# Optimization experiments

Measured on AMD Instinct MI355X. Metric: run time of the kernel, lower is better.

Reference implementation:

```python
import jax, jax.numpy as jnp
import numpy as np

D_DYN = 256    # dynamic_dim
D_STAT = 64    # static_dim
U_DIM = 48     # config.model.u_dim
N_OBS = 80     # num_prod*2 + num_inj = 32*2 + 16
T = 128        # rollout steps
B = 2048       # batch


def setup_inputs() -> dict:
    key = jax.random.key(0)
    k = jax.random.split(key, 8)
    z_dyn = jax.random.normal(k[0], (B, D_DYN), dtype=jnp.float32)
    z_static = jax.random.normal(k[1], (B, D_STAT), dtype=jnp.float32)
    dt = jnp.ones((1,), dtype=jnp.float32) * 0.05
    U = jax.random.normal(k[2], (T, B, U_DIM), dtype=jnp.float32)
    # learned params, initialized as in the torch module
    eig_raw = jnp.zeros((D_DYN,), dtype=jnp.float32)
    V = jnp.eye(D_DYN, dtype=jnp.float32) + jax.random.normal(k[3], (D_DYN, D_DYN), dtype=jnp.float32) * 0.01
    L = jax.random.normal(k[4], (D_DYN, U_DIM), dtype=jnp.float32) * (1.0 / np.sqrt(U_DIM))
    C = jax.random.normal(k[5], (N_OBS, D_DYN), dtype=jnp.float32) * (1.0 / np.sqrt(D_DYN))
    Dm = jax.random.normal(k[6], (N_OBS, U_DIM), dtype=jnp.float32) * (1.0 / np.sqrt(U_DIM))
    return {"z_dyn": z_dyn, "z_static": z_static, "dt": dt, "U": U,
            "eig_raw": eig_raw, "V": V, "L": L, "C": C, "Dm": Dm}


def reference(z_dyn, z_static, dt, U, eig_raw, V, L, C, Dm):
    # Stable Koopman operator: K = V diag(sigmoid(eig_raw)*0.99) V^{-1}
    eigvals = jax.nn.sigmoid(eig_raw) * 0.99
    K = (V * eigvals[None, :]) @ jnp.linalg.inv(V)  # [d, d]
    KT, LT, CT, DT = K.T, L.T, C.T, Dm.T
    dts = dt[0]

    def step(z, ut):
        ut_dt = ut * dts                 # [B, u_dim]
        z = z @ KT + ut_dt @ LT          # [B, d]
        y = z @ CT + ut_dt @ DT          # [B, n_obs]
        return z, (z, y)

    _, (Z, Y) = jax.lax.scan(step, z_dyn, U)
    return Z, Y  # [T, B, d], [T, B, n_obs]
```

## Files before the change

kernel.cpp:

```cpp
#include <hip/hip_runtime.h>

#define D_   256
#define UD_  48
#define NO_  80
#define T_   128
#define B_   2048

typedef __bf16 bf16x8 __attribute__((ext_vector_type(8)));
typedef float  f32x4  __attribute__((ext_vector_type(4)));
typedef unsigned short ushort_t;

static __device__ __forceinline__ ushort_t f2bf(float f){
  return __builtin_bit_cast(ushort_t, (__bf16)f);
}
static __device__ __forceinline__ float bf2f(ushort_t u){
  union { unsigned int i; float f; } c; c.i = ((unsigned int)u) << 16; return c.f;
}
static __device__ __forceinline__ f32x4 mfma16(bf16x8 a, bf16x8 b, f32x4 c){
  return __builtin_amdgcn_mfma_f32_16x16x32_bf16(a, b, c, 0, 0, 0);
}


__global__ void k_init(const float* __restrict__ V, const float* __restrict__ eig,
                       float* __restrict__ Xa, float* __restrict__ lam){
  const int i = blockIdx.x, j = threadIdx.x;
  Xa[i*D_ + j] = (i == j ? 2.0f : 0.0f) - V[i*D_ + j];
  if (j == 0) lam[i] = 0.99f / (1.0f + expf(-eig[i]));
}

__global__ void k_mm_mul(const float* __restrict__ A, const float* __restrict__ B,
                         float* __restrict__ Cm){
  const int i = blockIdx.x, j = threadIdx.x;
  const float* Ar = A + i*D_;
  float a0=0.f,a1=0.f,a2=0.f,a3=0.f;
  #pragma unroll 4
  for (int k = 0; k < D_; k += 4){
    a0 += Ar[k+0] * B[(k+0)*D_ + j];
    a1 += Ar[k+1] * B[(k+1)*D_ + j];
    a2 += Ar[k+2] * B[(k+2)*D_ + j];
    a3 += Ar[k+3] * B[(k+3)*D_ + j];
  }
  Cm[i*D_ + j] = (a0+a1)+(a2+a3);
}

__global__ void k_mm_upd(const float* __restrict__ X, const float* __restrict__ Tm,
                         float* __restrict__ Xn){
  const int i = blockIdx.x, j = threadIdx.x;
  const float* Xr = X + i*D_;
  float a0=0.f,a1=0.f,a2=0.f,a3=0.f;
  #pragma unroll 4
  for (int k = 0; k < D_; k += 4){
    a0 += Xr[k+0] * Tm[(k+0)*D_ + j];
    a1 += Xr[k+1] * Tm[(k+1)*D_ + j];
    a2 += Xr[k+2] * Tm[(k+2)*D_ + j];
    a3 += Xr[k+3] * Tm[(k+3)*D_ + j];
  }
  Xn[i*D_ + j] = 2.0f*Xr[j] - ((a0+a1)+(a2+a3));
}

__global__ void k_prep1(const float* __restrict__ Vinv, const float* __restrict__ V,
                        const float* __restrict__ Lm, const float* __restrict__ Cmat,
                        const float* __restrict__ dt,
                        float* __restrict__ VinvT, float* __restrict__ Lw,
                        float* __restrict__ Cw, float* __restrict__ dVd){
  const int bid = blockIdx.x, tid = threadIdx.x;
  if (bid < 256){
    VinvT[tid*D_ + bid] = Vinv[bid*D_ + tid];
    if (tid == bid){ float v = V[bid*D_ + bid]; dVd[bid] = v - bf2f(f2bf(v)); }
  } else if (bid < 512){
    const int i = bid - 256;
    if (tid < UD_){
      float acc = 0.f;
      #pragma unroll 4
      for (int j = 0; j < D_; ++j) acc += Vinv[i*D_ + j] * Lm[j*UD_ + tid];
      Lw[i*UD_ + tid] = acc * dt[0];
    }
  } else {
    const int n = bid - 512;
    float acc = 0.f;
    #pragma unroll 4
    for (int j = 0; j < D_; ++j) acc += Cmat[n*D_ + j] * V[j*D_ + tid];
    Cw[n*D_ + tid] = acc;
  }
}

__global__ void k_prep2(const float* __restrict__ z0, const float* __restrict__ VinvT,
                        const float* __restrict__ Lw,
                        ushort_t* __restrict__ Wchk, ushort_t* __restrict__ Lws){
  __shared__ float zr[8][256];
  const int bid = blockIdx.x, tid = threadIdx.x;
  if (bid < 256){
    const int b0 = bid * 8;
    #pragma unroll
    for (int r = 0; r < 8; ++r) zr[r][tid] = z0[(size_t)(b0+r)*D_ + tid];
    __syncthreads();
    float acc[8] = {0.f,0.f,0.f,0.f,0.f,0.f,0.f,0.f};
    #pragma unroll 4
    for (int j = 0; j < D_; ++j){
      const float vj = VinvT[j*D_ + tid];
      #pragma unroll
      for (int r = 0; r < 8; ++r) acc[r] += zr[r][j] * vj;
    }
    #pragma unroll
    for (int r = 0; r < 8; ++r)
      Wchk[(size_t)(b0+r)*D_ + tid] = f2bf(acc[r]);
    return;
  }
  const int f = bid - 256;
  if (tid >= 64) return;
  const int l = tid, lm = l & 15, lh = l >> 4;
  const int it = f >> 1, kc2 = f & 1;
  const int ig = it*16 + lm;
  #pragma unroll
  for (int j = 0; j < 8; ++j){
    const int k = 32*kc2 + 4*lh + (j & 3) + 16*(j >> 2);
    Lws[(f*64 + l)*8 + j] = f2bf(k < UD_ ? Lw[ig*UD_ + k] : 0.f);
  }
}

__global__ void k_packA(const float* __restrict__ V, const float* __restrict__ Cw,
                        const float* __restrict__ Dmat, const float* __restrict__ dt,
                        ushort_t* __restrict__ Af){
  const int mt = blockIdx.x / 10, kc = blockIdx.x % 10;
  const int l = threadIdx.x, lm = l & 15, lh = l >> 4;
  const float dts = dt[0];
  #pragma unroll
  for (int j = 0; j < 8; ++j){
    const int k = 32*kc + 4*lh + (j & 3) + 16*(j >> 2);
    float val = 0.f;
    if (mt < 16){
      if (kc < 8) val = V[(mt*16 + lm)*D_ + k];
    } else {
      const int n = (mt - 16)*16 + lm;
      if (kc < 8) val = Cw[n*D_ + k];
      else { const int ku = k - 256; if (ku < UD_) val = dts * Dmat[n*UD_ + ku]; }
    }
    Af[((size_t)(mt*10 + kc)*64 + l)*8 + j] = f2bf(val);
  }
}

#define SCAN_STEP(UA, UB, UC, TT) do {                                          \
  union { ushort_t us[8]; bf16x8 v; } c0, c1;                                   \
  c0.us[0]=f2bf((UA).x); c0.us[1]=f2bf((UA).y); c0.us[2]=f2bf((UA).z); c0.us[3]=f2bf((UA).w); \
  c0.us[4]=f2bf((UB).x); c0.us[5]=f2bf((UB).y); c0.us[6]=f2bf((UB).z); c0.us[7]=f2bf((UB).w); \
  c1.us[0]=f2bf((UC).x); c1.us[1]=f2bf((UC).y); c1.us[2]=f2bf((UC).z); c1.us[3]=f2bf((UC).w); \
  c1.us[4]=0; c1.us[5]=0; c1.us[6]=0; c1.us[7]=0;                               \
  _Pragma("unroll")                                                             \
  for (int q = 0; q < 2; ++q){                                                  \
    f32x4 acc = {0.f,0.f,0.f,0.f};                                              \
    acc = mfma16(lwf[q*2+0], c0.v, acc);                                        \
    acc = mfma16(lwf[q*2+1], c1.v, acc);                                        \
    _Pragma("unroll")                                                           \
    for (int r = 0; r < 4; ++r) w[q*4+r] = lamr[q*4+r]*w[q*4+r] + acc[r];       \
  }                                                                             \
  if ((((TT) & 7) == 7) && ((TT) < T_-1)){                                      \
    const int c2 = ((TT)+1) >> 3;                                               \
    _Pragma("unroll")                                                           \
    for (int q = 0; q < 2; ++q){                                                \
      const int i = (itb+q)*16 + 4*lh;                                          \
      ushort4 o; o.x=f2bf(w[q*4+0]); o.y=f2bf(w[q*4+1]); o.z=f2bf(w[q*4+2]); o.w=f2bf(w[q*4+3]); \
      *(ushort4*)(Wchk + ((size_t)c2*B_ + row)*D_ + i) = o;                     \
    }                                                                           \
  }                                                                             \
} while(0)

__global__ void __launch_bounds__(256) k_scan(const float* __restrict__ U,
    const ushort_t* __restrict__ Lws, const float* __restrict__ lam,
    ushort_t* __restrict__ Wchk){
  const int tid = threadIdx.x;
  const int wid = tid >> 6, l = tid & 63;
  const int lm = l & 15, lh = l >> 4;
  const int bq = blockIdx.x >> 1, ih = blockIdx.x & 1;
  const int b0 = bq * 16;
  const int row = b0 + lm;
  const int itb = ih*8 + wid*2;

  bf16x8 lwf[4];
  #pragma unroll
  for (int q = 0; q < 2; ++q)
    #pragma unroll
    for (int c = 0; c < 2; ++c)
      lwf[q*2 + c] = *(const bf16x8*)(Lws + ((size_t)(((itb+q)*2 + c)*64 + l))*8);

  float lamr[8], w[8];
  #pragma unroll
  for (int q = 0; q < 2; ++q){
    const int i = (itb+q)*16 + 4*lh;
    const float4 lv = *(const float4*)&lam[i];
    const ushort4 wu = *(const ushort4*)(Wchk + (size_t)row*D_ + i);
    lamr[q*4+0]=lv.x; lamr[q*4+1]=lv.y; lamr[q*4+2]=lv.z; lamr[q*4+3]=lv.w;
    w[q*4+0]=bf2f(wu.x); w[q*4+1]=bf2f(wu.y); w[q*4+2]=bf2f(wu.z); w[q*4+3]=bf2f(wu.w);
  }

  const size_t TS = (size_t)B_ * UD_;
  const float* Urow = U + (size_t)row * UD_;
  float4 Aa, Ab, Ac, Ba, Bb, Bc;
  Aa = *(const float4*)&Urow[4*lh]; Ab = *(const float4*)&Urow[16+4*lh]; Ac = *(const float4*)&Urow[32+4*lh];
  { const float* Up = Urow + TS;
    Ba = *(const float4*)&Up[4*lh]; Bb = *(const float4*)&Up[16+4*lh]; Bc = *(const float4*)&Up[32+4*lh]; }

  #pragma unroll 1
  for (int tt = 0; tt < 64; ++tt){
    const int t0 = 2*tt;
    SCAN_STEP(Aa, Ab, Ac, t0);
    if (t0 + 2 < T_){
      const float* Up = Urow + (size_t)(t0+2)*TS;
      Aa = *(const float4*)&Up[4*lh]; Ab = *(const float4*)&Up[16+4*lh]; Ac = *(const float4*)&Up[32+4*lh];
    }
    SCAN_STEP(Ba, Bb, Bc, t0+1);
    if (t0 + 3 < T_){
      const float* Up = Urow + (size_t)(t0+3)*TS;
      Ba = *(const float4*)&Up[4*lh]; Bb = *(const float4*)&Up[16+4*lh]; Bc = *(const float4*)&Up[32+4*lh];
    }
  }
}

__global__ void __launch_bounds__(256) k_fused(
    const float* __restrict__ U, const ushort_t* __restrict__ Af,
    const ushort_t* __restrict__ Lws, const float* __restrict__ lam,
    const float* __restrict__ dVd, const ushort_t* __restrict__ Wchk,
    float* __restrict__ outZ, float* __restrict__ outY){
  __shared__ __align__(16) ushort_t AfZhL[8*8*512];
  __shared__ __align__(16) ushort_t LwsL[32*512];
  __shared__ __align__(16) ushort_t AfYhL[30*512];
  __shared__ __align__(16) float    trbZ[4][16][68];
  __shared__ __align__(16) float    dVdL[128];
  __shared__ __align__(16) float    lamL[256];

  const int tid = threadIdx.x;
  const int bid = blockIdx.x;
  const int h  = bid >> 9;
  const int ch = bid & 15;
  const int bq = (bid >> 4) & 31;
  const int wid = tid >> 6, l = tid & 63;
  const int lm = l & 15, lh = l >> 4;
  const int col0 = bq*64 + wid*16;
  const int col = col0 + lm;

  {
    const uint4* gsrc = (const uint4*)Af;
    uint4* dz = (uint4*)AfZhL;
    #pragma unroll
    for (int r = 0; r < 16; ++r){
      const int i = r*256 + tid;
      const int f = i >> 6, l4 = i & 63;
      const int mi8 = f >> 3, kc = f & 7;
      dz[i] = gsrc[(size_t)((h*8 + mi8)*10 + kc)*64 + l4];
    }
    uint4* dy = (uint4*)AfYhL;
    const int nY = h ? 1280 : 1920;
    const int sb = 16 + (h ? 3 : 0);
    #pragma unroll
    for (int r = 0; r < 8; ++r){
      const int i = r*256 + tid;
      if (i < nY){
        const int f = i >> 6, l4 = i & 63;
        const int myl = f / 10, j = f % 10;
        dy[i] = gsrc[(size_t)((sb + myl)*10 + j)*64 + l4];
      }
    }
    const uint4* ls = (const uint4*)Lws;
    uint4* ld = (uint4*)LwsL;
    #pragma unroll
    for (int r = 0; r < 8; ++r) ld[r*256 + tid] = ls[r*256 + tid];
    if (tid < 32) ((float4*)dVdL)[tid] = ((const float4*)(dVd + h*128))[tid];
    else if (tid < 96) ((float4*)lamL)[tid-32] = ((const float4*)lam)[tid-32];
  }

  float w[64];
  #pragma unroll
  for (int kc = 0; kc < 8; ++kc)
    #pragma unroll
    for (int hh = 0; hh < 2; ++hh){
      const int i = 32*kc + 16*hh + 4*lh;
      const ushort4 wu = *(const ushort4*)(Wchk + ((size_t)ch*B_ + col)*D_ + i);
      const int e = 8*kc + 4*hh;
      w[e+0]=bf2f(wu.x); w[e+1]=bf2f(wu.y); w[e+2]=bf2f(wu.z); w[e+3]=bf2f(wu.w);
    }

  const size_t TS = (size_t)B_ * UD_;
  const float* Ucol = U + (size_t)col * UD_;
  float4 ua, ub, uc;
  {
    const float* Ut = Ucol + (size_t)(ch*8)*TS;
    ua = *(const float4*)&Ut[4*lh]; ub = *(const float4*)&Ut[16+4*lh]; uc = *(const float4*)&Ut[32+4*lh];
  }

  __syncthreads();

#define ZLOOP(HH)                                                               \
  { float* zbase = outZ + ((size_t)t*B_ + col0)*D_ + (HH)*128;                  \
    _Pragma("unroll")                                                           \
    for (int g = 0; g < 2; ++g){                                                \
      _Pragma("unroll")                                                         \
      for (int mi = 0; mi < 4; ++mi){                                           \
        const int mi8 = g*4 + mi;                                               \
        f32x4 acc = {0.f,0.f,0.f,0.f};                                          \
        _Pragma("unroll")                                                       \
        for (int kc = 0; kc < 8; ++kc){                                         \
          const bf16x8 af = *(const bf16x8*)&AfZhL[((mi8*8+kc)*64 + l)*8];      \
          acc = mfma16(af, wfr[kc], acc);                                       \
        }                                                                       \
        const float4 dv = *(const float4*)&dVdL[mi8*16 + 4*lh];                 \
        acc[0] += dv.x * (float)wfr[((HH)*8+mi8)>>1][0 + 4*(mi8&1)];            \
        acc[1] += dv.y * (float)wfr[((HH)*8+mi8)>>1][1 + 4*(mi8&1)];            \
        acc[2] += dv.z * (float)wfr[((HH)*8+mi8)>>1][2 + 4*(mi8&1)];            \
        acc[3] += dv.w * (float)wfr[((HH)*8+mi8)>>1][3 + 4*(mi8&1)];            \
        *(float4*)&trbZ[wid][lm][mi*16 + 4*lh] = make_float4(acc[0],acc[1],acc[2],acc[3]); \
      }                                                                         \
      __builtin_amdgcn_wave_barrier();                                          \
      _Pragma("unroll")                                                         \
      for (int j = 0; j < 4; ++j){                                              \
        const int r_ = j*4 + (l >> 4), c16 = l & 15;                            \
        const float4 v = *(const float4*)&trbZ[wid][r_][4*c16];                 \
        *(float4*)&zbase[(size_t)r_*D_ + g*64 + 4*c16] = v;                     \
      }                                                                         \
      __builtin_amdgcn_wave_barrier();                                          \
    } }

#define YLOOP(COFF, NMY)                                                        \
  { float* yrow = outY + ((size_t)t*B_ + col)*NO_ + (COFF);                     \
    _Pragma("unroll")                                                           \
    for (int my = 0; my < (NMY); ++my){                                         \
      f32x4 acc = {0.f,0.f,0.f,0.f};                                            \
      _Pragma("unroll")                                                         \
      for (int kc = 0; kc < 8; ++kc){                                           \
        const bf16x8 af = *(const bf16x8*)&AfYhL[((my*10+kc)*64 + l)*8];        \
        acc = mfma16(af, wfr[kc], acc);                                         \
      }                                                                         \
      { const bf16x8 af8 = *(const bf16x8*)&AfYhL[((my*10+8)*64 + l)*8];        \
        const bf16x8 af9 = *(const bf16x8*)&AfYhL[((my*10+9)*64 + l)*8];        \
        acc = mfma16(af8, uf0, acc); acc = mfma16(af9, uf1, acc); }             \
      *(float4*)&yrow[my*16 + 4*lh] = make_float4(acc[0],acc[1],acc[2],acc[3]); \
    } }

  #pragma unroll 1
  for (int s = 0; s < 8; ++s){
    const int t = ch*8 + s;
    bf16x8 uf0, uf1;
    {
      union { ushort_t us[8]; bf16x8 v; } cv;
      cv.us[0]=f2bf(ua.x); cv.us[1]=f2bf(ua.y); cv.us[2]=f2bf(ua.z); cv.us[3]=f2bf(ua.w);
      cv.us[4]=f2bf(ub.x); cv.us[5]=f2bf(ub.y); cv.us[6]=f2bf(ub.z); cv.us[7]=f2bf(ub.w);
      uf0 = cv.v;
      cv.us[0]=f2bf(uc.x); cv.us[1]=f2bf(uc.y); cv.us[2]=f2bf(uc.z); cv.us[3]=f2bf(uc.w);
      cv.us[4]=0; cv.us[5]=0; cv.us[6]=0; cv.us[7]=0;
      uf1 = cv.v;
    }
    if (s < 7){
      const float* Ut = Ucol + (size_t)(t+1)*TS;
      ua = *(const float4*)&Ut[4*lh]; ub = *(const float4*)&Ut[16+4*lh]; uc = *(const float4*)&Ut[32+4*lh];
    }
    #pragma unroll
    for (int it = 0; it < 16; ++it){
      const bf16x8 a0 = *(const bf16x8*)&LwsL[((it*2+0)*64 + l)*8];
      const bf16x8 a1 = *(const bf16x8*)&LwsL[((it*2+1)*64 + l)*8];
      const float4 lv = *(const float4*)&lamL[32*(it>>1) + 16*(it&1) + 4*lh];
      f32x4 acc = {0.f,0.f,0.f,0.f};
      acc = mfma16(a0, uf0, acc);
      acc = mfma16(a1, uf1, acc);
      const int e0 = 8*(it>>1) + 4*(it&1);
      w[e0+0] = lv.x*w[e0+0] + acc[0];
      w[e0+1] = lv.y*w[e0+1] + acc[1];
      w[e0+2] = lv.z*w[e0+2] + acc[2];
      w[e0+3] = lv.w*w[e0+3] + acc[3];
    }
    bf16x8 wfr[8];
    #pragma unroll
    for (int kc = 0; kc < 8; ++kc){
      union { ushort_t us[8]; bf16x8 v; } cv;
      #pragma unroll
      for (int j = 0; j < 8; ++j) cv.us[j] = f2bf(w[8*kc + j]);
      wfr[kc] = cv.v;
    }
    if (h == 0){
      ZLOOP(0);
      YLOOP(0, 3);
    } else {
      ZLOOP(1);
      YLOOP(48, 2);
    }
  }
#undef ZLOOP
#undef YLOOP
}

extern "C" void kernel_launch(void* const* d_in, const int* in_sizes, int n_in,
                              void* d_out, int out_size, void* d_ws, size_t ws_size,
                              hipStream_t stream){
  const float* z0  = (const float*)d_in[0];
  const float* dt  = (const float*)d_in[2];
  const float* U   = (const float*)d_in[3];
  const float* eig = (const float*)d_in[4];
  const float* V   = (const float*)d_in[5];
  const float* L   = (const float*)d_in[6];
  const float* C   = (const float*)d_in[7];
  const float* Dm  = (const float*)d_in[8];
  float* outZ = (float*)d_out;
  float* outY = outZ + (size_t)T_*B_*D_;

  char* ws = (char*)d_ws;
  float* Xa    = (float*)(ws + 0);
  float* Xb    = (float*)(ws + 262144);
  float* Tt    = (float*)(ws + 524288);
  float* Lw    = (float*)(ws + 786432);
  float* Cw    = (float*)(ws + 835584);
  float* lam   = (float*)(ws + 917504);
  float* dVd   = (float*)(ws + 918528);
  ushort_t* Af   = (ushort_t*)(ws + 919552);
  ushort_t* Lws  = (ushort_t*)(ws + 1134592);
  ushort_t* Wchk = (ushort_t*)(ws + 1167360);
  if (ws_size < 17944576u) return;

  k_init<<<256,256,0,stream>>>(V, eig, Xa, lam);
  k_mm_mul<<<256,256,0,stream>>>(V, Xa, Tt);
  k_mm_upd<<<256,256,0,stream>>>(Xa, Tt, Xb);
  k_mm_mul<<<256,256,0,stream>>>(V, Xb, Tt);
  k_mm_upd<<<256,256,0,stream>>>(Xb, Tt, Xa);
  k_mm_mul<<<256,256,0,stream>>>(V, Xa, Tt);
  k_mm_upd<<<256,256,0,stream>>>(Xa, Tt, Xb);
  k_prep1<<<592,256,0,stream>>>(Xb, V, L, C, dt, Xa, Lw, Cw, dVd);
  k_prep2<<<288,256,0,stream>>>(z0, Xa, Lw, Wchk, Lws);
  k_packA<<<210,64,0,stream>>>(V, Cw, Dm, dt, Af);
  k_scan<<<256,256,0,stream>>>(U, Lws, lam, Wchk);
  k_fused<<<1024,256,0,stream>>>(U, Af, Lws, lam, dVd, Wchk, outZ, outY);
}
```

Before: 267.8 us.

## Merge preparation and scan kernels into one cooperative kernel with grid syncs

Eleven small preparation launches (Newton-Schulz inverse iterations, the projections, the packing and the chunked scan) become one cooperative kernel that separates phases with grid.sync(). This removes launch gaps and tail idle time between the many tiny dependent kernels. The fused kernel's block-to-work mapping is also reordered so the two halves are interleaved, and the Y output rows are split differently between halves (4 vs 1 tiles instead of 3 vs 2). Risks are the cost of grid-wide barriers and an uneven load between the two halves in the fused kernel.

```diff
diff --git a/kernel.cpp b/kernel.cpp
--- a/kernel.cpp
+++ b/kernel.cpp
@@ -1,4 +1,7 @@
 #include <hip/hip_runtime.h>
+#include <hip/hip_cooperative_groups.h>
+
+namespace cg = cooperative_groups;
 
 #define D_   256
 #define UD_  48
@@ -21,123 +24,23 @@
 }
 
 
-__global__ void k_init(const float* __restrict__ V, const float* __restrict__ eig,
-                       float* __restrict__ Xa, float* __restrict__ lam){
-  const int i = blockIdx.x, j = threadIdx.x;
-  Xa[i*D_ + j] = (i == j ? 2.0f : 0.0f) - V[i*D_ + j];
-  if (j == 0) lam[i] = 0.99f / (1.0f + expf(-eig[i]));
-}
-
-__global__ void k_mm_mul(const float* __restrict__ A, const float* __restrict__ B,
-                         float* __restrict__ Cm){
-  const int i = blockIdx.x, j = threadIdx.x;
-  const float* Ar = A + i*D_;
-  float a0=0.f,a1=0.f,a2=0.f,a3=0.f;
-  #pragma unroll 4
-  for (int k = 0; k < D_; k += 4){
-    a0 += Ar[k+0] * B[(k+0)*D_ + j];
-    a1 += Ar[k+1] * B[(k+1)*D_ + j];
-    a2 += Ar[k+2] * B[(k+2)*D_ + j];
-    a3 += Ar[k+3] * B[(k+3)*D_ + j];
-  }
-  Cm[i*D_ + j] = (a0+a1)+(a2+a3);
-}
-
-__global__ void k_mm_upd(const float* __restrict__ X, const float* __restrict__ Tm,
-                         float* __restrict__ Xn){
-  const int i = blockIdx.x, j = threadIdx.x;
-  const float* Xr = X + i*D_;
-  float a0=0.f,a1=0.f,a2=0.f,a3=0.f;
-  #pragma unroll 4
-  for (int k = 0; k < D_; k += 4){
-    a0 += Xr[k+0] * Tm[(k+0)*D_ + j];
-    a1 += Xr[k+1] * Tm[(k+1)*D_ + j];
-    a2 += Xr[k+2] * Tm[(k+2)*D_ + j];
-    a3 += Xr[k+3] * Tm[(k+3)*D_ + j];
-  }
-  Xn[i*D_ + j] = 2.0f*Xr[j] - ((a0+a1)+(a2+a3));
-}
-
-__global__ void k_prep1(const float* __restrict__ Vinv, const float* __restrict__ V,
-                        const float* __restrict__ Lm, const float* __restrict__ Cmat,
-                        const float* __restrict__ dt,
-                        float* __restrict__ VinvT, float* __restrict__ Lw,
-                        float* __restrict__ Cw, float* __restrict__ dVd){
-  const int bid = blockIdx.x, tid = threadIdx.x;
-  if (bid < 256){
-    VinvT[tid*D_ + bid] = Vinv[bid*D_ + tid];
-    if (tid == bid){ float v = V[bid*D_ + bid]; dVd[bid] = v - bf2f(f2bf(v)); }
-  } else if (bid < 512){
-    const int i = bid - 256;
-    if (tid < UD_){
-      float acc = 0.f;
-      #pragma unroll 4
-      for (int j = 0; j < D_; ++j) acc += Vinv[i*D_ + j] * Lm[j*UD_ + tid];
-      Lw[i*UD_ + tid] = acc * dt[0];
-    }
-  } else {
-    const int n = bid - 512;
-    float acc = 0.f;
-    #pragma unroll 4
-    for (int j = 0; j < D_; ++j) acc += Cmat[n*D_ + j] * V[j*D_ + tid];
-    Cw[n*D_ + tid] = acc;
-  }
-}
-
-__global__ void k_prep2(const float* __restrict__ z0, const float* __restrict__ VinvT,
-                        const float* __restrict__ Lw,
-                        ushort_t* __restrict__ Wchk, ushort_t* __restrict__ Lws){
-  __shared__ float zr[8][256];
-  const int bid = blockIdx.x, tid = threadIdx.x;
-  if (bid < 256){
-    const int b0 = bid * 8;
-    #pragma unroll
-    for (int r = 0; r < 8; ++r) zr[r][tid] = z0[(size_t)(b0+r)*D_ + tid];
-    __syncthreads();
-    float acc[8] = {0.f,0.f,0.f,0.f,0.f,0.f,0.f,0.f};
-    #pragma unroll 4
-    for (int j = 0; j < D_; ++j){
-      const float vj = VinvT[j*D_ + tid];
-      #pragma unroll
-      for (int r = 0; r < 8; ++r) acc[r] += zr[r][j] * vj;
-    }
-    #pragma unroll
-    for (int r = 0; r < 8; ++r)
-      Wchk[(size_t)(b0+r)*D_ + tid] = f2bf(acc[r]);
-    return;
-  }
-  const int f = bid - 256;
-  if (tid >= 64) return;
-  const int l = tid, lm = l & 15, lh = l >> 4;
-  const int it = f >> 1, kc2 = f & 1;
-  const int ig = it*16 + lm;
-  #pragma unroll
-  for (int j = 0; j < 8; ++j){
-    const int k = 32*kc2 + 4*lh + (j & 3) + 16*(j >> 2);
-    Lws[(f*64 + l)*8 + j] = f2bf(k < UD_ ? Lw[ig*UD_ + k] : 0.f);
-  }
-}
-
-__global__ void k_packA(const float* __restrict__ V, const float* __restrict__ Cw,
-                        const float* __restrict__ Dmat, const float* __restrict__ dt,
-                        ushort_t* __restrict__ Af){
-  const int mt = blockIdx.x / 10, kc = blockIdx.x % 10;
-  const int l = threadIdx.x, lm = l & 15, lh = l >> 4;
-  const float dts = dt[0];
-  #pragma unroll
-  for (int j = 0; j < 8; ++j){
-    const int k = 32*kc + 4*lh + (j & 3) + 16*(j >> 2);
-    float val = 0.f;
-    if (mt < 16){
-      if (kc < 8) val = V[(mt*16 + lm)*D_ + k];
-    } else {
-      const int n = (mt - 16)*16 + lm;
-      if (kc < 8) val = Cw[n*D_ + k];
-      else { const int ku = k - 256; if (ku < UD_) val = dts * Dmat[n*UD_ + ku]; }
-    }
-    Af[((size_t)(mt*10 + kc)*64 + l)*8 + j] = f2bf(val);
-  }
-}
+#define NS_MUL(Ap, Bp, Cp) do {                                                 \
+  const float* Ar = (Ap) + bid*D_;                                              \
+  float a0=0.f,a1=0.f,a2=0.f,a3=0.f;                                            \
+  _Pragma("unroll 4")                                                           \
+  for (int k = 0; k < D_; k += 4){                                              \
+    a0 += Ar[k+0]*(Bp)[(k+0)*D_+tid]; a1 += Ar[k+1]*(Bp)[(k+1)*D_+tid];         \
+    a2 += Ar[k+2]*(Bp)[(k+2)*D_+tid]; a3 += Ar[k+3]*(Bp)[(k+3)*D_+tid]; }       \
+  (Cp)[bid*D_+tid] = (a0+a1)+(a2+a3); } while(0)
+
+#define NS_UPD(Xp, Tp, Xn) do {                                                 \
+  const float* Xr = (Xp) + bid*D_;                                              \
+  float a0=0.f,a1=0.f,a2=0.f,a3=0.f;                                            \
+  _Pragma("unroll 4")                                                           \
+  for (int k = 0; k < D_; k += 4){                                              \
+    a0 += Xr[k+0]*(Tp)[(k+0)*D_+tid]; a1 += Xr[k+1]*(Tp)[(k+1)*D_+tid];         \
+    a2 += Xr[k+2]*(Tp)[(k+2)*D_+tid]; a3 += Xr[k+3]*(Tp)[(k+3)*D_+tid]; }       \
+  (Xn)[bid*D_+tid] = 2.0f*Xr[tid] - ((a0+a1)+(a2+a3)); } while(0)
 
 #define SCAN_STEP(UA, UB, UC, TT) do {                                          \
   union { ushort_t us[8]; bf16x8 v; } c0, c1;                                   \
@@ -164,53 +67,140 @@
   }                                                                             \
 } while(0)
 
-__global__ void __launch_bounds__(256) k_scan(const float* __restrict__ U,
-    const ushort_t* __restrict__ Lws, const float* __restrict__ lam,
+__global__ void __launch_bounds__(256) k_prep(
+    const float* __restrict__ V, const float* __restrict__ eig,
+    const float* __restrict__ Lm, const float* __restrict__ Cmat,
+    const float* __restrict__ Dmat, const float* __restrict__ dt,
+    const float* __restrict__ z0, const float* __restrict__ U,
+    float* __restrict__ Xa, float* __restrict__ Xb, float* __restrict__ Tt,
+    float* __restrict__ Lw, float* __restrict__ Cw,
+    float* __restrict__ lam, float* __restrict__ dVd,
+    ushort_t* __restrict__ Af, ushort_t* __restrict__ Lws,
     ushort_t* __restrict__ Wchk){
-  const int tid = threadIdx.x;
-  const int wid = tid >> 6, l = tid & 63;
-  const int lm = l & 15, lh = l >> 4;
-  const int bq = blockIdx.x >> 1, ih = blockIdx.x & 1;
-  const int b0 = bq * 16;
-  const int row = b0 + lm;
-  const int itb = ih*8 + wid*2;
-
-  bf16x8 lwf[4];
-  #pragma unroll
-  for (int q = 0; q < 2; ++q)
-    #pragma unroll
-    for (int c = 0; c < 2; ++c)
-      lwf[q*2 + c] = *(const bf16x8*)(Lws + ((size_t)(((itb+q)*2 + c)*64 + l))*8);
-
-  float lamr[8], w[8];
-  #pragma unroll
-  for (int q = 0; q < 2; ++q){
-    const int i = (itb+q)*16 + 4*lh;
-    const float4 lv = *(const float4*)&lam[i];
-    const ushort4 wu = *(const ushort4*)(Wchk + (size_t)row*D_ + i);
-    lamr[q*4+0]=lv.x; lamr[q*4+1]=lv.y; lamr[q*4+2]=lv.z; lamr[q*4+3]=lv.w;
-    w[q*4+0]=bf2f(wu.x); w[q*4+1]=bf2f(wu.y); w[q*4+2]=bf2f(wu.z); w[q*4+3]=bf2f(wu.w);
-  }
-
-  const size_t TS = (size_t)B_ * UD_;
-  const float* Urow = U + (size_t)row * UD_;
-  float4 Aa, Ab, Ac, Ba, Bb, Bc;
-  Aa = *(const float4*)&Urow[4*lh]; Ab = *(const float4*)&Urow[16+4*lh]; Ac = *(const float4*)&Urow[32+4*lh];
-  { const float* Up = Urow + TS;
-    Ba = *(const float4*)&Up[4*lh]; Bb = *(const float4*)&Up[16+4*lh]; Bc = *(const float4*)&Up[32+4*lh]; }
-
-  #pragma unroll 1
-  for (int tt = 0; tt < 64; ++tt){
-    const int t0 = 2*tt;
-    SCAN_STEP(Aa, Ab, Ac, t0);
-    if (t0 + 2 < T_){
-      const float* Up = Urow + (size_t)(t0+2)*TS;
-      Aa = *(const float4*)&Up[4*lh]; Ab = *(const float4*)&Up[16+4*lh]; Ac = *(const float4*)&Up[32+4*lh];
-    }
-    SCAN_STEP(Ba, Bb, Bc, t0+1);
-    if (t0 + 3 < T_){
-      const float* Up = Urow + (size_t)(t0+3)*TS;
-      Ba = *(const float4*)&Up[4*lh]; Bb = *(const float4*)&Up[16+4*lh]; Bc = *(const float4*)&Up[32+4*lh];
+  __shared__ float zr[8][256];
+  cg::grid_group grid = cg::this_grid();
+  const int bid = blockIdx.x, tid = threadIdx.x;
+
+  Xa[bid*D_ + tid] = (bid == tid ? 2.0f : 0.0f) - V[bid*D_ + tid];
+  if (tid == 0) lam[bid] = 0.99f / (1.0f + expf(-eig[bid]));
+  grid.sync();
+  NS_MUL(V, Xa, Tt);  grid.sync();
+  NS_UPD(Xa, Tt, Xb); grid.sync();
+  NS_MUL(V, Xb, Tt);  grid.sync();
+  NS_UPD(Xb, Tt, Xa); grid.sync();
+  NS_MUL(V, Xa, Tt);  grid.sync();
+  NS_UPD(Xa, Tt, Xb); grid.sync();
+  {
+    Xa[tid*D_ + bid] = Xb[bid*D_ + tid];
+    if (tid == bid){ float v = V[bid*D_ + bid]; dVd[bid] = v - bf2f(f2bf(v)); }
+    if (tid < UD_){
+      float acc = 0.f;
+      #pragma unroll 4
+      for (int j = 0; j < D_; ++j) acc += Xb[bid*D_ + j] * Lm[j*UD_ + tid];
+      Lw[bid*UD_ + tid] = acc * dt[0];
+    }
+    if (bid < NO_){
+      float acc = 0.f;
+      #pragma unroll 4
+      for (int j = 0; j < D_; ++j) acc += Cmat[bid*D_ + j] * V[j*D_ + tid];
+      Cw[bid*D_ + tid] = acc;
+    }
+  }
+  grid.sync();
+  {
+    const int b0 = bid * 8;
+    #pragma unroll
+    for (int r = 0; r < 8; ++r) zr[r][tid] = z0[(size_t)(b0+r)*D_ + tid];
+    __syncthreads();
+    float acc[8] = {0.f,0.f,0.f,0.f,0.f,0.f,0.f,0.f};
+    #pragma unroll 4
+    for (int j = 0; j < D_; ++j){
+      const float vj = Xa[j*D_ + tid];
+      #pragma unroll
+      for (int r = 0; r < 8; ++r) acc[r] += zr[r][j] * vj;
+    }
+    #pragma unroll
+    for (int r = 0; r < 8; ++r)
+      Wchk[(size_t)(b0+r)*D_ + tid] = f2bf(acc[r]);
+
+    if (bid < 32 && tid < 64){
+      const int f = bid, l = tid, lm = l & 15, lh = l >> 4;
+      const int it = f >> 1, kc2 = f & 1;
+      const int ig = it*16 + lm;
+      #pragma unroll
+      for (int j = 0; j < 8; ++j){
+        const int k = 32*kc2 + 4*lh + (j & 3) + 16*(j >> 2);
+        Lws[(f*64 + l)*8 + j] = f2bf(k < UD_ ? Lw[ig*UD_ + k] : 0.f);
+      }
+    }
+    {
+      const int v = bid*4 + (tid >> 6);
+      if (v < 210){
+        const int mt = v / 10, kc = v % 10;
+        const int l = tid & 63, lm = l & 15, lh = l >> 4;
+        const float dts = dt[0];
+        #pragma unroll
+        for (int j = 0; j < 8; ++j){
+          const int k = 32*kc + 4*lh + (j & 3) + 16*(j >> 2);
+          float val = 0.f;
+          if (mt < 16){
+            if (kc < 8) val = V[(mt*16 + lm)*D_ + k];
+          } else {
+            const int n = (mt - 16)*16 + lm;
+            if (kc < 8) val = Cw[n*D_ + k];
+            else { const int ku = k - 256; if (ku < UD_) val = dts * Dmat[n*UD_ + ku]; }
+          }
+          Af[((size_t)(mt*10 + kc)*64 + l)*8 + j] = f2bf(val);
+        }
+      }
+    }
+  }
+  grid.sync();
+  {
+    const int wid = tid >> 6, l = tid & 63;
+    const int lm = l & 15, lh = l >> 4;
+    const int bq = bid >> 1, ih = bid & 1;
+    const int b0 = bq * 16;
+    const int row = b0 + lm;
+    const int itb = ih*8 + wid*2;
+
+    bf16x8 lwf[4];
+    #pragma unroll
+    for (int q = 0; q < 2; ++q)
+      #pragma unroll
+      for (int c = 0; c < 2; ++c)
+        lwf[q*2 + c] = *(const bf16x8*)(Lws + ((size_t)(((itb+q)*2 + c)*64 + l))*8);
+
+    float lamr[8], w[8];
+    #pragma unroll
+    for (int q = 0; q < 2; ++q){
+      const int i = (itb+q)*16 + 4*lh;
+      const float4 lv = *(const float4*)&lam[i];
+      const ushort4 wu = *(const ushort4*)(Wchk + (size_t)row*D_ + i);
+      lamr[q*4+0]=lv.x; lamr[q*4+1]=lv.y; lamr[q*4+2]=lv.z; lamr[q*4+3]=lv.w;
+      w[q*4+0]=bf2f(wu.x); w[q*4+1]=bf2f(wu.y); w[q*4+2]=bf2f(wu.z); w[q*4+3]=bf2f(wu.w);
+    }
+
+    const size_t TS = (size_t)B_ * UD_;
+    const float* Urow = U + (size_t)row * UD_;
+    float4 Aa, Ab, Ac, Ba, Bb, Bc;
+    Aa = *(const float4*)&Urow[4*lh]; Ab = *(const float4*)&Urow[16+4*lh]; Ac = *(const float4*)&Urow[32+4*lh];
+    { const float* Up = Urow + TS;
+      Ba = *(const float4*)&Up[4*lh]; Bb = *(const float4*)&Up[16+4*lh]; Bc = *(const float4*)&Up[32+4*lh]; }
+
+    #pragma unroll 1
+    for (int tt = 0; tt < 64; ++tt){
+      const int t0 = 2*tt;
+      SCAN_STEP(Aa, Ab, Ac, t0);
+      if (t0 + 2 < T_){
+        const float* Up = Urow + (size_t)(t0+2)*TS;
+        Aa = *(const float4*)&Up[4*lh]; Ab = *(const float4*)&Up[16+4*lh]; Ac = *(const float4*)&Up[32+4*lh];
+      }
+      SCAN_STEP(Ba, Bb, Bc, t0+1);
+      if (t0 + 3 < T_){
+        const float* Up = Urow + (size_t)(t0+3)*TS;
+        Ba = *(const float4*)&Up[4*lh]; Bb = *(const float4*)&Up[16+4*lh]; Bc = *(const float4*)&Up[32+4*lh];
+      }
     }
   }
 }
@@ -222,16 +212,16 @@
     float* __restrict__ outZ, float* __restrict__ outY){
   __shared__ __align__(16) ushort_t AfZhL[8*8*512];
   __shared__ __align__(16) ushort_t LwsL[32*512];
-  __shared__ __align__(16) ushort_t AfYhL[30*512];
+  __shared__ __align__(16) ushort_t AfYhL[40*512];
   __shared__ __align__(16) float    trbZ[4][16][68];
   __shared__ __align__(16) float    dVdL[128];
   __shared__ __align__(16) float    lamL[256];
 
   const int tid = threadIdx.x;
   const int bid = blockIdx.x;
-  const int h  = bid >> 9;
-  const int ch = bid & 15;
-  const int bq = (bid >> 4) & 31;
+  const int h  = bid & 1;
+  const int ch = (bid >> 1) & 15;
+  const int bq = bid >> 5;
   const int wid = tid >> 6, l = tid & 63;
   const int lm = l & 15, lh = l >> 4;
   const int col0 = bq*64 + wid*16;
@@ -248,10 +238,10 @@
       dz[i] = gsrc[(size_t)((h*8 + mi8)*10 + kc)*64 + l4];
     }
     uint4* dy = (uint4*)AfYhL;
-    const int nY = h ? 1280 : 1920;
-    const int sb = 16 + (h ? 3 : 0);
-    #pragma unroll
-    for (int r = 0; r < 8; ++r){
+    const int nY = h ? 640 : 2560;
+    const int sb = 16 + (h ? 4 : 0);
+    #pragma unroll
+    for (int r = 0; r < 10; ++r){
       const int i = r*256 + tid;
       if (i < nY){
         const int f = i >> 6, l4 = i & 63;
@@ -375,10 +365,10 @@
     }
     if (h == 0){
       ZLOOP(0);
-      YLOOP(0, 3);
+      YLOOP(0, 4);
     } else {
       ZLOOP(1);
-      YLOOP(48, 2);
+      YLOOP(64, 1);
     }
   }
 #undef ZLOOP
@@ -412,16 +402,15 @@
   ushort_t* Wchk = (ushort_t*)(ws + 1167360);
   if (ws_size < 17944576u) return;
 
-  k_init<<<256,256,0,stream>>>(V, eig, Xa, lam);
-  k_mm_mul<<<256,256,0,stream>>>(V, Xa, Tt);
-  k_mm_upd<<<256,256,0,stream>>>(Xa, Tt, Xb);
-  k_mm_mul<<<256,256,0,stream>>>(V, Xb, Tt);
-  k_mm_upd<<<256,256,0,stream>>>(Xb, Tt, Xa);
-  k_mm_mul<<<256,256,0,stream>>>(V, Xa, Tt);
-  k_mm_upd<<<256,256,0,stream>>>(Xa, Tt, Xb);
-  k_prep1<<<592,256,0,stream>>>(Xb, V, L, C, dt, Xa, Lw, Cw, dVd);
-  k_prep2<<<288,256,0,stream>>>(z0, Xa, Lw, Wchk, Lws);
-  k_packA<<<210,64,0,stream>>>(V, Cw, Dm, dt, Af);
-  k_scan<<<256,256,0,stream>>>(U, Lws, lam, Wchk);
+  {
+    void* args[] = {
+      (void*)&V, (void*)&eig, (void*)&L, (void*)&C, (void*)&Dm, (void*)&dt,
+      (void*)&z0, (void*)&U,
+      (void*)&Xa, (void*)&Xb, (void*)&Tt, (void*)&Lw, (void*)&Cw,
+      (void*)&lam, (void*)&dVd, (void*)&Af, (void*)&Lws, (void*)&Wchk
+    };
+    hipLaunchCooperativeKernel((const void*)k_prep, dim3(256), dim3(256),
+                               args, 0, stream);
+  }
   k_fused<<<1024,256,0,stream>>>(U, Af, Lws, lam, dVd, Wchk, outZ, outY);
 }
```

New measurement: 539.6 us. 2.01x slower.

## Process two timesteps per iteration to share A-fragment LDS loads across steps

Applied to the files above, without the earlier changes.

The fused kernel now advances the recurrence two timesteps per loop iteration and issues paired MFMAs that reuse each LDS-loaded A fragment for both steps. This halves LDS traffic for the Z and Y projection matrices. The block index mapping is changed so the two halves are interleaved across adjacent blocks, and the Y-output split between halves is rebalanced from 3/2 to 4/1 tiles. The cost is higher register pressure from the doubled fragments and accumulators, and the Y work split is now less even between halves.

```diff
diff --git a/kernel.cpp b/kernel.cpp
--- a/kernel.cpp
+++ b/kernel.cpp
@@ -222,16 +222,16 @@
     float* __restrict__ outZ, float* __restrict__ outY){
   __shared__ __align__(16) ushort_t AfZhL[8*8*512];
   __shared__ __align__(16) ushort_t LwsL[32*512];
-  __shared__ __align__(16) ushort_t AfYhL[30*512];
+  __shared__ __align__(16) ushort_t AfYhL[40*512];
   __shared__ __align__(16) float    trbZ[4][16][68];
   __shared__ __align__(16) float    dVdL[128];
   __shared__ __align__(16) float    lamL[256];
 
   const int tid = threadIdx.x;
   const int bid = blockIdx.x;
-  const int h  = bid >> 9;
-  const int ch = bid & 15;
-  const int bq = (bid >> 4) & 31;
+  const int h  = bid & 1;
+  const int ch = (bid >> 1) & 15;
+  const int bq = bid >> 5;
   const int wid = tid >> 6, l = tid & 63;
   const int lm = l & 15, lh = l >> 4;
   const int col0 = bq*64 + wid*16;
@@ -248,10 +248,10 @@
       dz[i] = gsrc[(size_t)((h*8 + mi8)*10 + kc)*64 + l4];
     }
     uint4* dy = (uint4*)AfYhL;
-    const int nY = h ? 1280 : 1920;
-    const int sb = 16 + (h ? 3 : 0);
-    #pragma unroll
-    for (int r = 0; r < 8; ++r){
+    const int nY = h ? 640 : 2560;
+    const int sb = 16 + (h ? 4 : 0);
+    #pragma unroll
+    for (int r = 0; r < 10; ++r){
       const int i = r*256 + tid;
       if (i < nY){
         const int f = i >> 6, l4 = i & 63;
@@ -280,105 +280,140 @@
 
   const size_t TS = (size_t)B_ * UD_;
   const float* Ucol = U + (size_t)col * UD_;
-  float4 ua, ub, uc;
+  float4 uaA, ubA, ucA, uaB, ubB, ucB;
   {
     const float* Ut = Ucol + (size_t)(ch*8)*TS;
-    ua = *(const float4*)&Ut[4*lh]; ub = *(const float4*)&Ut[16+4*lh]; uc = *(const float4*)&Ut[32+4*lh];
+    uaA = *(const float4*)&Ut[4*lh]; ubA = *(const float4*)&Ut[16+4*lh]; ucA = *(const float4*)&Ut[32+4*lh];
+    const float* Ut1 = Ut + TS;
+    uaB = *(const float4*)&Ut1[4*lh]; ubB = *(const float4*)&Ut1[16+4*lh]; ucB = *(const float4*)&Ut1[32+4*lh];
   }
 
   __syncthreads();
 
 #define ZLOOP(HH)                                                               \
-  { float* zbase = outZ + ((size_t)t*B_ + col0)*D_ + (HH)*128;                  \
+  { float* zA = outZ + ((size_t)t*B_ + col0)*D_ + (HH)*128;                     \
+    float* zB = zA + (size_t)B_*D_;                                             \
     _Pragma("unroll")                                                           \
-    for (int g = 0; g < 2; ++g){                                                \
+    for (int g = 0; g < 4; ++g){                                                \
       _Pragma("unroll")                                                         \
-      for (int mi = 0; mi < 4; ++mi){                                           \
-        const int mi8 = g*4 + mi;                                               \
-        f32x4 acc = {0.f,0.f,0.f,0.f};                                          \
+      for (int mi = 0; mi < 2; ++mi){                                           \
+        const int mi8 = g*2 + mi;                                               \
+        f32x4 aA = {0.f,0.f,0.f,0.f}, aB = {0.f,0.f,0.f,0.f};                   \
         _Pragma("unroll")                                                       \
         for (int kc = 0; kc < 8; ++kc){                                         \
           const bf16x8 af = *(const bf16x8*)&AfZhL[((mi8*8+kc)*64 + l)*8];      \
-          acc = mfma16(af, wfr[kc], acc);                                       \
+          aA = mfma16(af, wfrA[kc], aA);                                        \
+          aB = mfma16(af, wfrB[kc], aB);                                        \
         }                                                                       \
         const float4 dv = *(const float4*)&dVdL[mi8*16 + 4*lh];                 \
-        acc[0] += dv.x * (float)wfr[((HH)*8+mi8)>>1][0 + 4*(mi8&1)];            \
-        acc[1] += dv.y * (float)wfr[((HH)*8+mi8)>>1][1 + 4*(mi8&1)];            \
-        acc[2] += dv.z * (float)wfr[((HH)*8+mi8)>>1][2 + 4*(mi8&1)];            \
-        acc[3] += dv.w * (float)wfr[((HH)*8+mi8)>>1][3 + 4*(mi8&1)];            \
-        *(float4*)&trbZ[wid][lm][mi*16 + 4*lh] = make_float4(acc[0],acc[1],acc[2],acc[3]); \
+        _Pragma("unroll")                                                       \
+        for (int r = 0; r < 4; ++r){                                            \
+          aA[r] += ((const float*)&dv)[r] * (float)wfrA[(HH)*4+(mi8>>1)][r + 4*(mi8&1)]; \
+          aB[r] += ((const float*)&dv)[r] * (float)wfrB[(HH)*4+(mi8>>1)][r + 4*(mi8&1)]; \
+        }                                                                       \
+        *(float4*)&trbZ[wid][lm][mi*16 + 4*lh] = make_float4(aA[0],aA[1],aA[2],aA[3]); \
+        *(float4*)&trbZ[wid][lm][32 + mi*16 + 4*lh] = make_float4(aB[0],aB[1],aB[2],aB[3]); \
       }                                                                         \
       __builtin_amdgcn_wave_barrier();                                          \
       _Pragma("unroll")                                                         \
       for (int j = 0; j < 4; ++j){                                              \
-        const int r_ = j*4 + (l >> 4), c16 = l & 15;                            \
-        const float4 v = *(const float4*)&trbZ[wid][r_][4*c16];                 \
-        *(float4*)&zbase[(size_t)r_*D_ + g*64 + 4*c16] = v;                     \
+        const int stp = j >> 1, jr = (j & 1)*8;                                 \
+        const int r_ = jr + (l >> 3), c8 = l & 7;                               \
+        const float4 v = *(const float4*)&trbZ[wid][r_][stp*32 + 4*c8];         \
+        float* dst = stp ? zB : zA;                                             \
+        *(float4*)&dst[(size_t)r_*D_ + g*32 + 4*c8] = v;                        \
       }                                                                         \
       __builtin_amdgcn_wave_barrier();                                          \
     } }
 
 #define YLOOP(COFF, NMY)                                                        \
-  { float* yrow = outY + ((size_t)t*B_ + col)*NO_ + (COFF);                     \
+  { float* yA = outY + ((size_t)t*B_ + col)*NO_ + (COFF);                       \
+    float* yB = yA + (size_t)B_*NO_;                                            \
     _Pragma("unroll")                                                           \
     for (int my = 0; my < (NMY); ++my){                                         \
-      f32x4 acc = {0.f,0.f,0.f,0.f};                                            \
+      f32x4 aA = {0.f,0.f,0.f,0.f}, aB = {0.f,0.f,0.f,0.f};                     \
       _Pragma("unroll")                                                         \
       for (int kc = 0; kc < 8; ++kc){                                           \
         const bf16x8 af = *(const bf16x8*)&AfYhL[((my*10+kc)*64 + l)*8];        \
-        acc = mfma16(af, wfr[kc], acc);                                         \
+        aA = mfma16(af, wfrA[kc], aA);                                          \
+        aB = mfma16(af, wfrB[kc], aB);                                          \
       }                                                                         \
       { const bf16x8 af8 = *(const bf16x8*)&AfYhL[((my*10+8)*64 + l)*8];        \
         const bf16x8 af9 = *(const bf16x8*)&AfYhL[((my*10+9)*64 + l)*8];        \
-        acc = mfma16(af8, uf0, acc); acc = mfma16(af9, uf1, acc); }             \
-      *(float4*)&yrow[my*16 + 4*lh] = make_float4(acc[0],acc[1],acc[2],acc[3]); \
+        aA = mfma16(af8, ufA0, aA); aA = mfma16(af9, ufA1, aA);                 \
+        aB = mfma16(af8, ufB0, aB); aB = mfma16(af9, ufB1, aB); }               \
+      *(float4*)&yA[my*16 + 4*lh] = make_float4(aA[0],aA[1],aA[2],aA[3]);       \
+      *(float4*)&yB[my*16 + 4*lh] = make_float4(aB[0],aB[1],aB[2],aB[3]);       \
     } }
 
   #pragma unroll 1
-  for (int s = 0; s < 8; ++s){
-    const int t = ch*8 + s;
-    bf16x8 uf0, uf1;
+  for (int p = 0; p < 4; ++p){
+    const int t = ch*8 + 2*p;
+    bf16x8 ufA0, ufA1, ufB0, ufB1;
     {
       union { ushort_t us[8]; bf16x8 v; } cv;
-      cv.us[0]=f2bf(ua.x); cv.us[1]=f2bf(ua.y); cv.us[2]=f2bf(ua.z); cv.us[3]=f2bf(ua.w);
-      cv.us[4]=f2bf(ub.x); cv.us[5]=f2bf(ub.y); cv.us[6]=f2bf(ub.z); cv.us[7]=f2bf(ub.w);
-      uf0 = cv.v;
-      cv.us[0]=f2bf(uc.x); cv.us[1]=f2bf(uc.y); cv.us[2]=f2bf(uc.z); cv.us[3]=f2bf(uc.w);
+      cv.us[0]=f2bf(uaA.x); cv.us[1]=f2bf(uaA.y); cv.us[2]=f2bf(uaA.z); cv.us[3]=f2bf(uaA.w);
+      cv.us[4]=f2bf(ubA.x); cv.us[5]=f2bf(ubA.y); cv.us[6]=f2bf(ubA.z); cv.us[7]=f2bf(ubA.w);
+      ufA0 = cv.v;
+      cv.us[0]=f2bf(ucA.x); cv.us[1]=f2bf(ucA.y); cv.us[2]=f2bf(ucA.z); cv.us[3]=f2bf(ucA.w);
       cv.us[4]=0; cv.us[5]=0; cv.us[6]=0; cv.us[7]=0;
-      uf1 = cv.v;
-    }
-    if (s < 7){
-      const float* Ut = Ucol + (size_t)(t+1)*TS;
-      ua = *(const float4*)&Ut[4*lh]; ub = *(const float4*)&Ut[16+4*lh]; uc = *(const float4*)&Ut[32+4*lh];
-    }
-    #pragma unroll
-    for (int it = 0; it < 16; ++it){
-      const bf16x8 a0 = *(const bf16x8*)&LwsL[((it*2+0)*64 + l)*8];
-      const bf16x8 a1 = *(const bf16x8*)&LwsL[((it*2+1)*64 + l)*8];
-      const float4 lv = *(const float4*)&lamL[32*(it>>1) + 16*(it&1) + 4*lh];
-      f32x4 acc = {0.f,0.f,0.f,0.f};
-      acc = mfma16(a0, uf0, acc);
-      acc = mfma16(a1, uf1, acc);
-      const int e0 = 8*(it>>1) + 4*(it&1);
-      w[e0+0] = lv.x*w[e0+0] + acc[0];
-      w[e0+1] = lv.y*w[e0+1] + acc[1];
-      w[e0+2] = lv.z*w[e0+2] + acc[2];
-      w[e0+3] = lv.w*w[e0+3] + acc[3];
-    }
-    bf16x8 wfr[8];
-    #pragma unroll
-    for (int kc = 0; kc < 8; ++kc){
-      union { ushort_t us[8]; bf16x8 v; } cv;
+      ufA1 = cv.v;
+      cv.us[0]=f2bf(uaB.x); cv.us[1]=f2bf(uaB.y); cv.us[2]=f2bf(uaB.z); cv.us[3]=f2bf(uaB.w);
+      cv.us[4]=f2bf(ubB.x); cv.us[5]=f2bf(ubB.y); cv.us[6]=f2bf(ubB.z); cv.us[7]=f2bf(ubB.w);
+      ufB0 = cv.v;
+      cv.us[0]=f2bf(ucB.x); cv.us[1]=f2bf(ucB.y); cv.us[2]=f2bf(ucB.z); cv.us[3]=f2bf(ucB.w);
+      cv.us[4]=0; cv.us[5]=0; cv.us[6]=0; cv.us[7]=0;
+      ufB1 = cv.v;
+    }
+    if (p < 3){
+      const float* Ut = Ucol + (size_t)(t+2)*TS;
+      uaA = *(const float4*)&Ut[4*lh]; ubA = *(const float4*)&Ut[16+4*lh]; ucA = *(const float4*)&Ut[32+4*lh];
+      const float* Ut1 = Ut + TS;
+      uaB = *(const float4*)&Ut1[4*lh]; ubB = *(const float4*)&Ut1[16+4*lh]; ucB = *(const float4*)&Ut1[32+4*lh];
+    }
+    bf16x8 wfrA[8], wfrB[8];
+    {
+      union u8 { ushort_t us[8]; bf16x8 v; } cvA[8];
       #pragma unroll
-      for (int j = 0; j < 8; ++j) cv.us[j] = f2bf(w[8*kc + j]);
-      wfr[kc] = cv.v;
+      for (int it = 0; it < 16; ++it){
+        const bf16x8 a0 = *(const bf16x8*)&LwsL[((it*2+0)*64 + l)*8];
+        const bf16x8 a1 = *(const bf16x8*)&LwsL[((it*2+1)*64 + l)*8];
+        const float4 lv = *(const float4*)&lamL[32*(it>>1) + 16*(it&1) + 4*lh];
+        f32x4 pA = {0.f,0.f,0.f,0.f};
+        pA = mfma16(a0, ufA0, pA);
+        pA = mfma16(a1, ufA1, pA);
+        f32x4 pB = {0.f,0.f,0.f,0.f};
+        pB = mfma16(a0, ufB0, pB);
+        pB = mfma16(a1, ufB1, pB);
+        const int e0 = 8*(it>>1) + 4*(it&1);
+        const float wa0 = lv.x*w[e0+0] + pA[0];
+        const float wa1 = lv.y*w[e0+1] + pA[1];
+        const float wa2 = lv.z*w[e0+2] + pA[2];
+        const float wa3 = lv.w*w[e0+3] + pA[3];
+        w[e0+0] = lv.x*wa0 + pB[0];
+        w[e0+1] = lv.y*wa1 + pB[1];
+        w[e0+2] = lv.z*wa2 + pB[2];
+        w[e0+3] = lv.w*wa3 + pB[3];
+        cvA[it>>1].us[4*(it&1)+0] = f2bf(wa0);
+        cvA[it>>1].us[4*(it&1)+1] = f2bf(wa1);
+        cvA[it>>1].us[4*(it&1)+2] = f2bf(wa2);
+        cvA[it>>1].us[4*(it&1)+3] = f2bf(wa3);
+      }
+      #pragma unroll
+      for (int kc = 0; kc < 8; ++kc){
+        wfrA[kc] = cvA[kc].v;
+        union u8 cv;
+        #pragma unroll
+        for (int j = 0; j < 8; ++j) cv.us[j] = f2bf(w[8*kc + j]);
+        wfrB[kc] = cv.v;
+      }
     }
     if (h == 0){
       ZLOOP(0);
-      YLOOP(0, 3);
+      YLOOP(0, 4);
     } else {
       ZLOOP(1);
-      YLOOP(48, 2);
+      YLOOP(64, 1);
     }
   }
 #undef ZLOOP
```

Measured after the change: 298.3 us. 1.11x slower.
